# Kernel optimization log

Measured on AMD Instinct MI355X. Metric: run time of the kernel, lower is better.

## Reference

```python
import jax, jax.numpy as jnp
import numpy as np

B, CIN, COUT, S1, S2, M1, M2 = 16, 64, 64, 128, 128, 16, 16


def _cas(L, dtype):
    # Hartley 'cas' matrix: cos(2*pi*k*k'/L) + sin(2*pi*k*k'/L), symmetric LxL
    k = jnp.arange(L, dtype=dtype)
    ang = (2.0 * jnp.pi / L) * (k[:, None] * k[None, :])
    return jnp.cos(ang) + jnp.sin(ang)


def dht2(x):
    # x: [B, C, M, N] -> dense 2D discrete Hartley transform via matmuls
    M, N = x.shape[-2], x.shape[-1]
    cas_row = _cas(M, x.dtype)
    cas_col = _cas(N, x.dtype)
    # torch: matmul(x, cas_col.T) then matmul(cas_row.T, .)
    y = jnp.einsum('bimn,gn->bimg', x, cas_col)
    return jnp.einsum('mf,bimn->bifn', cas_row, y)


def idht2(x):
    return dht2(x) / (x.shape[-2] * x.shape[-1])


def _neg_freq(a):
    # roll(flip(a, [-1,-2]), (1,1), [-1,-2])
    return jnp.roll(jnp.flip(a, axis=(-2, -1)), shift=(1, 1), axis=(-2, -1))


def compl_mul2d(x1, x2):
    x1n = _neg_freq(x1)
    x2n = _neg_freq(x2)
    e = lambda a, b: jnp.einsum('bixy,ioxy->boxy', a, b)
    return 0.5 * (e(x1, x2) - e(x1n, x2n) + e(x1, x2n) + e(x1n, x2))


def setup_inputs() -> dict:
    key = jax.random.key(0)
    k1, k2, k3 = jax.random.split(key, 3)
    scale = 1.0 / (CIN * COUT)
    x = jax.random.normal(k1, (B, CIN, S1, S2), dtype=jnp.float32)
    weights1 = scale * jax.random.uniform(k2, (CIN, COUT, M1, M2), dtype=jnp.float32)
    weights2 = scale * jax.random.uniform(k3, (CIN, COUT, M1, M2), dtype=jnp.float32)
    return {'x': x, 'weights1': weights1, 'weights2': weights2}


def reference(x, weights1, weights2):
    m1, m2 = weights1.shape[2], weights1.shape[3]
    b, cout = x.shape[0], weights1.shape[1]
    s1, s2 = x.shape[-2], x.shape[-1]

    cos_part = dht2(x)
    sin_part = dht2(jnp.flip(x, axis=(-2, -1)))
    # torch.angle(complex(cos, sin)) == atan2(sin, cos)
    phase = jnp.arctan2(sin_part, cos_part)

    out_dht = jnp.zeros((b, cout, s1, s2), dtype=x.dtype)
    out_dht = out_dht.at[:, :, :m1, :m2].set(
        compl_mul2d(cos_part[:, :, :m1, :m2], weights1))
    out_dht = out_dht.at[:, :, -m1:, :m2].set(
        compl_mul2d(cos_part[:, :, -m1:, :m2], weights2))

    y = idht2(out_dht)
    return y * jnp.cos(phase)
```

## Files before the change

kernel.cpp:

```cpp
#include <hip/hip_runtime.h>

typedef _Float16 f16;
typedef f16 f16x4 __attribute__((ext_vector_type(4)));
typedef f16 f16x8 __attribute__((ext_vector_type(8)));
typedef float f32x4 __attribute__((ext_vector_type(4)));

#define LSCALE 2048.0f
#define LINV   4.8828125e-4f
#define XSX 136
#define XSW 140

#define MFMA(A,B,C) __builtin_amdgcn_mfma_f32_16x16x32_f16(A, B, C, 0, 0, 0)

__device__ __forceinline__ int frag_slot(int row, int k) {
    return ((((row >> 4) * 4 + (k >> 5)) * 64) + ((k >> 3) & 3) * 16 + (row & 15)) * 8 + (k & 7);
}

__global__ void k_cas(float* __restrict__ casf,
                      f16* __restrict__ FAh, f16* __restrict__ FAl,
                      f16* __restrict__ FVh, f16* __restrict__ FVl) {
    int f = blockIdx.x, m = threadIdx.x;
    const float SC = (float)(6.283185307179586 / 128.0);
    float ang = SC * (float)(f * m);
    double a = (double)ang;
    float v = (float)cos(a) + (float)sin(a);
    casf[f * 128 + m] = v;
    f16 h = (f16)v;
    f16 lo = (f16)((v - (float)h) * LSCALE);
    int sA = frag_slot(f, m);
    FAh[sA] = h;
    FAl[sA] = lo;
    int sV = frag_slot(f, 127 - m);
    FVh[sV] = h;
    FVl[sV] = lo;
}

__global__ __launch_bounds__(512, 2) void k_dht(
    const float* __restrict__ xg,
    const f16* __restrict__ FAh, const f16* __restrict__ FAl,
    const f16* __restrict__ FVh, const f16* __restrict__ FVl,
    float* __restrict__ outbuf,
    float* __restrict__ cp1, float* __restrict__ cp2)
{
    __shared__ __align__(16) char smem[71680];
    f16* Xh  = (f16*)smem;
    f16* Xl  = (f16*)(smem + 34816);
    f16* W1h = (f16*)smem;
    f16* W1l = (f16*)(smem + 17920);
    f16* W2h = (f16*)(smem + 35840);
    f16* W2l = (f16*)(smem + 53760);

    const int img = blockIdx.x;
    const int gh  = blockIdx.y;
    const float* X = xg + (size_t)img * 16384;
    const int t = threadIdx.x;
    const int lane = t & 63;
    const int wv = t >> 6;
    const int l15 = lane & 15;
    const int a4 = lane >> 4;

    #pragma unroll
    for (int it = 0; it < 8; ++it) {
        int i = it * 512 + t;
        int r = i >> 5, c0 = (i & 31) * 4;
        float4 xv = *(const float4*)&X[r * 128 + c0];
        const float* xp = (const float*)&xv;
        f16x4 hv, lv;
        #pragma unroll
        for (int j = 0; j < 4; ++j) {
            f16 h = (f16)xp[j];
            hv[j] = h;
            lv[j] = (f16)((xp[j] - (float)h) * LSCALE);
        }
        *(f16x4*)&Xh[r * XSX + c0] = hv;
        *(f16x4*)&Xl[r * XSX + c0] = lv;
    }
    __syncthreads();

    const int gq = wv >> 2, mq = wv & 3;
    const int Gq = 2 * gh + gq;
    f32x4 w1hi[2][2], w1lo[2][2], w2hi[2][2], w2lo[2][2];
    #pragma unroll
    for (int i = 0; i < 2; ++i)
        #pragma unroll
        for (int j = 0; j < 2; ++j) {
            w1hi[i][j] = (f32x4){0.f,0.f,0.f,0.f}; w1lo[i][j] = (f32x4){0.f,0.f,0.f,0.f};
            w2hi[i][j] = (f32x4){0.f,0.f,0.f,0.f}; w2lo[i][j] = (f32x4){0.f,0.f,0.f,0.f};
        }
    {
        #pragma unroll 1
        for (int ks = 0; ks < 4; ++ks) {
            f16x8 tah[2], tal[2], tvh[2], tvl[2];
            #pragma unroll
            for (int gt = 0; gt < 2; ++gt) {
                const int toff = (((2 * Gq + gt) * 4 + ks) * 64 + lane) * 8;
                tah[gt] = *(const f16x8*)&FAh[toff];
                tal[gt] = *(const f16x8*)&FAl[toff];
                tvh[gt] = *(const f16x8*)&FVh[toff];
                tvl[gt] = *(const f16x8*)&FVl[toff];
            }
            #pragma unroll
            for (int mt = 0; mt < 2; ++mt) {
                const int base = (32 * mq + 16 * mt + l15) * XSX + ks * 32 + 8 * a4;
                f16x8 xh = *(const f16x8*)&Xh[base];
                f16x8 xl = *(const f16x8*)&Xl[base];
                #pragma unroll
                for (int gt = 0; gt < 2; ++gt) {
                    w1hi[gt][mt] = MFMA(tah[gt], xh, w1hi[gt][mt]);
                    w1lo[gt][mt] = MFMA(tal[gt], xh, w1lo[gt][mt]);
                    w1lo[gt][mt] = MFMA(tah[gt], xl, w1lo[gt][mt]);
                    w2hi[gt][mt] = MFMA(tvh[gt], xh, w2hi[gt][mt]);
                    w2lo[gt][mt] = MFMA(tvl[gt], xh, w2lo[gt][mt]);
                    w2lo[gt][mt] = MFMA(tvh[gt], xl, w2lo[gt][mt]);
                }
            }
        }
    }
    __syncthreads();

    {
        #pragma unroll
        for (int gt = 0; gt < 2; ++gt)
            #pragma unroll
            for (int mt = 0; mt < 2; ++mt) {
                const int m = 32 * mq + 16 * mt + l15;
                #pragma unroll
                for (int r = 0; r < 4; ++r) {
                    const int g = 32 * gq + 16 * gt + 4 * a4 + r;
                    float v1 = w1hi[gt][mt][r] + LINV * w1lo[gt][mt][r];
                    f16 h1 = (f16)v1;
                    float v2 = w2hi[gt][mt][r] + LINV * w2lo[gt][mt][r];
                    f16 h2 = (f16)v2;
                    W2h[g * XSW + m] = h2;
                    W2l[g * XSW + m] = (f16)((v2 - (float)h2) * LSCALE);
                    W1h[g * XSW + m] = h1;
                    W1l[g * XSW + m] = (f16)((v1 - (float)h1) * LSCALE);
                }
            }
    }
    __syncthreads();

    const int fq = wv >> 1, gq2 = wv & 1;
    f32x4 chi[2][2], clo[2][2], shi[2][2], slo[2][2];
    #pragma unroll
    for (int i = 0; i < 2; ++i)
        #pragma unroll
        for (int j = 0; j < 2; ++j) {
            chi[i][j] = (f32x4){0.f,0.f,0.f,0.f}; clo[i][j] = (f32x4){0.f,0.f,0.f,0.f};
            shi[i][j] = (f32x4){0.f,0.f,0.f,0.f}; slo[i][j] = (f32x4){0.f,0.f,0.f,0.f};
        }
    {
        #pragma unroll 1
        for (int ks = 0; ks < 4; ++ks) {
            f16x8 tah[2], tal[2], tvh[2], tvl[2];
            #pragma unroll
            for (int ft = 0; ft < 2; ++ft) {
                const int toff = (((2 * fq + ft) * 4 + ks) * 64 + lane) * 8;
                tah[ft] = *(const f16x8*)&FAh[toff];
                tal[ft] = *(const f16x8*)&FAl[toff];
                tvh[ft] = *(const f16x8*)&FVh[toff];
                tvl[ft] = *(const f16x8*)&FVl[toff];
            }
            #pragma unroll
            for (int gt = 0; gt < 2; ++gt) {
                const int wb = (32 * gq2 + 16 * gt + l15) * XSW + ks * 32 + 8 * a4;
                f16x4 a0 = *(const f16x4*)&W1h[wb];
                f16x4 a1 = *(const f16x4*)&W1h[wb + 4];
                f16x4 b0 = *(const f16x4*)&W1l[wb];
                f16x4 b1 = *(const f16x4*)&W1l[wb + 4];
                f16x4 c0 = *(const f16x4*)&W2h[wb];
                f16x4 c1 = *(const f16x4*)&W2h[wb + 4];
                f16x4 d0 = *(const f16x4*)&W2l[wb];
                f16x4 d1 = *(const f16x4*)&W2l[wb + 4];
                f16x8 u1h = __builtin_shufflevector(a0, a1, 0,1,2,3,4,5,6,7);
                f16x8 u1l = __builtin_shufflevector(b0, b1, 0,1,2,3,4,5,6,7);
                f16x8 u2h = __builtin_shufflevector(c0, c1, 0,1,2,3,4,5,6,7);
                f16x8 u2l = __builtin_shufflevector(d0, d1, 0,1,2,3,4,5,6,7);
                #pragma unroll
                for (int ft = 0; ft < 2; ++ft) {
                    chi[ft][gt] = MFMA(tah[ft], u1h, chi[ft][gt]);
                    clo[ft][gt] = MFMA(tal[ft], u1h, clo[ft][gt]);
                    clo[ft][gt] = MFMA(tah[ft], u1l, clo[ft][gt]);
                    shi[ft][gt] = MFMA(tvh[ft], u2h, shi[ft][gt]);
                    slo[ft][gt] = MFMA(tvl[ft], u2h, slo[ft][gt]);
                    slo[ft][gt] = MFMA(tvh[ft], u2l, slo[ft][gt]);
                }
            }
        }
    }

    f16* cph = (f16*)(outbuf + (size_t)img * 16384);
    #pragma unroll
    for (int ft = 0; ft < 2; ++ft)
        #pragma unroll
        for (int gt = 0; gt < 2; ++gt) {
            const int g = 64 * gh + 32 * gq2 + 16 * gt + l15;
            #pragma unroll
            for (int r = 0; r < 4; ++r) {
                const int f = 32 * fq + 16 * ft + 4 * a4 + r;
                float Cv = chi[ft][gt][r] + LINV * clo[ft][gt][r];
                float Sv = shi[ft][gt][r] + LINV * slo[ft][gt][r];
                float d = Cv * Cv + Sv * Sv;
                float cp = (d > 0.f) ? Cv * rsqrtf(d) : 1.0f;
                cph[f * 128 + g] = (f16)cp;
                if (gh == 0 && gq2 == 0 && gt == 0) {
                    if (fq == 0 && ft == 0)
                        cp1[img * 256 + f * 16 + l15] = Cv;
                    else if (fq == 3 && ft == 1)
                        cp2[img * 256 + (f - 112) * 16 + l15] = Cv;
                }
            }
        }
}

__global__ __launch_bounds__(256) void k_inv(
    const float* __restrict__ cp1, const float* __restrict__ cp2,
    const float* __restrict__ w1,  const float* __restrict__ w2,
    const float* __restrict__ cas,
    float* __restrict__ out)
{
    __shared__ float odS[32 * 16];
    __shared__ float casF[128 * 33];
    __shared__ float Rs[128 * 17];
    __shared__ float casG[16 * 128];

    const int img = blockIdx.x;
    const int b = img >> 6, o = img & 63;
    const int t = threadIdx.x;
    const int grp = t >> 5, lane = t & 31;
    const int s2 = lane * 4;

    const f16* phg = (const f16*)(out + (size_t)img * 16384);
    f16x4 phv[16];
    #pragma unroll
    for (int r = 0; r < 16; ++r)
        phv[r] = *(const f16x4*)&phg[(grp * 16 + r) * 128 + s2];

    {
        const int xx = t >> 4, yy = t & 15;
        const int nx = (16 - xx) & 15, ny = (16 - yy) & 15;
        const int pf = xx * 16 + yy, pn = nx * 16 + ny;
        float a1p = 0.f, a1m = 0.f, a2p = 0.f, a2m = 0.f;
        #pragma unroll 4
        for (int i = 0; i < 64; ++i) {
            const int cb = (b * 64 + i) * 256;
            const int wb = (i * 64 + o) * 256;
            float A1  = cp1[cb + pf];
            float A1n = cp1[cb + pn];
            float W1v = w1[wb + pf];
            float W1n = w1[wb + pn];
            a1p = fmaf(A1,  W1v + W1n, a1p);
            a1m = fmaf(A1n, W1v - W1n, a1m);
            float A2  = cp2[cb + pf];
            float A2n = cp2[cb + pn];
            float W2v = w2[wb + pf];
            float W2n = w2[wb + pn];
            a2p = fmaf(A2,  W2v + W2n, a2p);
            a2m = fmaf(A2n, W2v - W2n, a2m);
        }
        odS[pf]       = 0.5f * (a1p + a1m);
        odS[256 + pf] = 0.5f * (a2p + a2m);
    }

    #pragma unroll
    for (int k = 0; k < 16; ++k) {
        int idx = t + k * 256;
        int s = idx >> 5, j = idx & 31;
        int f = (j < 16) ? j : (96 + j);
        casF[s * 33 + j] = cas[s * 128 + f];
    }
    #pragma unroll
    for (int k = 0; k < 8; ++k) {
        int idx = t + k * 256;
        casG[idx] = cas[idx];
    }
    __syncthreads();

    {
        const int s1 = t >> 1, gb = (t & 1) * 8;
        float acc[8];
        #pragma unroll
        for (int l = 0; l < 8; ++l) acc[l] = 0.f;
        #pragma unroll 4
        for (int j = 0; j < 32; ++j) {
            float cf = casF[s1 * 33 + j];
            #pragma unroll
            for (int l = 0; l < 8; ++l)
                acc[l] = fmaf(cf, odS[j * 16 + gb + l], acc[l]);
        }
        #pragma unroll
        for (int l = 0; l < 8; ++l) Rs[s1 * 17 + gb + l] = acc[l];
    }
    __syncthreads();

    const float inv = 1.0f / 16384.0f;
    #pragma unroll
    for (int r = 0; r < 16; ++r) {
        const int s1 = grp * 16 + r;
        float4 acc = {0.f, 0.f, 0.f, 0.f};
        #pragma unroll
        for (int g = 0; g < 16; ++g) {
            float rv = Rs[s1 * 17 + g];
            float4 c4 = *(const float4*)&casG[g * 128 + s2];
            acc.x = fmaf(rv, c4.x, acc.x);
            acc.y = fmaf(rv, c4.y, acc.y);
            acc.z = fmaf(rv, c4.z, acc.z);
            acc.w = fmaf(rv, c4.w, acc.w);
        }
        size_t idx = (size_t)img * 16384 + (size_t)s1 * 128 + s2;
        float4 res;
        res.x = acc.x * inv * (float)phv[r][0];
        res.y = acc.y * inv * (float)phv[r][1];
        res.z = acc.z * inv * (float)phv[r][2];
        res.w = acc.w * inv * (float)phv[r][3];
        *(float4*)&out[idx] = res;
    }
}

extern "C" void kernel_launch(void* const* d_in, const int* in_sizes, int n_in,
                              void* d_out, int out_size, void* d_ws, size_t ws_size,
                              hipStream_t stream) {
    (void)in_sizes; (void)n_in; (void)out_size; (void)ws_size;
    const float* x  = (const float*)d_in[0];
    const float* w1 = (const float*)d_in[1];
    const float* w2 = (const float*)d_in[2];
    float* out = (float*)d_out;
    float* ws  = (float*)d_ws;

    float* casf = ws;
    f16* FAh = (f16*)(ws + 16384);
    f16* FAl = FAh + 16384;
    f16* FVh = FAl + 16384;
    f16* FVl = FVh + 16384;
    float* cp1 = (float*)(FVl + 16384);
    float* cp2 = cp1 + 262144;

    k_cas<<<dim3(128), dim3(128), 0, stream>>>(casf, FAh, FAl, FVh, FVl);
    k_dht<<<dim3(1024, 2), dim3(512), 0, stream>>>(x, FAh, FAl, FVh, FVl, out, cp1, cp2);
    k_inv<<<dim3(1024), dim3(256), 0, stream>>>(cp1, cp2, w1, w2, casf, out);
}
```

Before: 150.5 us.

## Store pre-negated frequency copies and vectorise spectral mixing with warp specialisation

Result: slower. 164.1 us (+9.0%).

```diff
diff --git a/kernel.cpp b/kernel.cpp
--- a/kernel.cpp
+++ b/kernel.cpp
@@ -40,7 +40,8 @@
     const f16* __restrict__ FAh, const f16* __restrict__ FAl,
     const f16* __restrict__ FVh, const f16* __restrict__ FVl,
     float* __restrict__ outbuf,
-    float* __restrict__ cp1, float* __restrict__ cp2)
+    float* __restrict__ cp1, float* __restrict__ cp2,
+    float* __restrict__ cp1n, float* __restrict__ cp2n)
 {
     __shared__ __align__(16) char smem[71680];
     f16* Xh  = (f16*)smem;
@@ -204,10 +205,15 @@
                 float cp = (d > 0.f) ? Cv * rsqrtf(d) : 1.0f;
                 cph[f * 128 + g] = (f16)cp;
                 if (gh == 0 && gq2 == 0 && gt == 0) {
-                    if (fq == 0 && ft == 0)
+                    const int gn = (16 - l15) & 15;
+                    if (fq == 0 && ft == 0) {
                         cp1[img * 256 + f * 16 + l15] = Cv;
-                    else if (fq == 3 && ft == 1)
-                        cp2[img * 256 + (f - 112) * 16 + l15] = Cv;
+                        cp1n[img * 256 + ((16 - f) & 15) * 16 + gn] = Cv;
+                    } else if (fq == 3 && ft == 1) {
+                        const int fl = f - 112;
+                        cp2[img * 256 + fl * 16 + l15] = Cv;
+                        cp2n[img * 256 + ((16 - fl) & 15) * 16 + gn] = Cv;
+                    }
                 }
             }
         }
@@ -215,6 +221,7 @@
 
 __global__ __launch_bounds__(256) void k_inv(
     const float* __restrict__ cp1, const float* __restrict__ cp2,
+    const float* __restrict__ cp1n, const float* __restrict__ cp2n,
     const float* __restrict__ w1,  const float* __restrict__ w2,
     const float* __restrict__ cas,
     float* __restrict__ out)
@@ -236,43 +243,58 @@
     for (int r = 0; r < 16; ++r)
         phv[r] = *(const f16x4*)&phg[(grp * 16 + r) * 128 + s2];
 
-    {
-        const int xx = t >> 4, yy = t & 15;
-        const int nx = (16 - xx) & 15, ny = (16 - yy) & 15;
-        const int pf = xx * 16 + yy, pn = nx * 16 + ny;
-        float a1p = 0.f, a1m = 0.f, a2p = 0.f, a2m = 0.f;
+    if (t < 128) {
+        const int c  = t >> 6;
+        const int s  = t & 63;
+        const int xx = s >> 2;
+        const int yb = (s & 3) * 4;
+        const int pix = xx * 16 + yb;
+        const int nx = (16 - xx) & 15;
+        const int nlo = nx * 16 + (12 - yb);
+        const int nup = nx * 16 + ((16 - yb) & 15);
+        const float* cp  = c ? cp2  : cp1;
+        const float* cpn = c ? cp2n : cp1n;
+        const float* w   = c ? w2   : w1;
+        float4 accp = {0.f,0.f,0.f,0.f}, accm = {0.f,0.f,0.f,0.f};
         #pragma unroll 4
         for (int i = 0; i < 64; ++i) {
             const int cb = (b * 64 + i) * 256;
             const int wb = (i * 64 + o) * 256;
-            float A1  = cp1[cb + pf];
-            float A1n = cp1[cb + pn];
-            float W1v = w1[wb + pf];
-            float W1n = w1[wb + pn];
-            a1p = fmaf(A1,  W1v + W1n, a1p);
-            a1m = fmaf(A1n, W1v - W1n, a1m);
-            float A2  = cp2[cb + pf];
-            float A2n = cp2[cb + pn];
-            float W2v = w2[wb + pf];
-            float W2n = w2[wb + pn];
-            a2p = fmaf(A2,  W2v + W2n, a2p);
-            a2m = fmaf(A2n, W2v - W2n, a2m);
-        }
-        odS[pf]       = 0.5f * (a1p + a1m);
-        odS[256 + pf] = 0.5f * (a2p + a2m);
-    }
-
-    #pragma unroll
-    for (int k = 0; k < 16; ++k) {
-        int idx = t + k * 256;
-        int s = idx >> 5, j = idx & 31;
-        int f = (j < 16) ? j : (96 + j);
-        casF[s * 33 + j] = cas[s * 128 + f];
-    }
-    #pragma unroll
-    for (int k = 0; k < 8; ++k) {
-        int idx = t + k * 256;
-        casG[idx] = cas[idx];
+            float4 A4  = *(const float4*)&cp[cb + pix];
+            float4 An4 = *(const float4*)&cpn[cb + pix];
+            float4 W4  = *(const float4*)&w[wb + pix];
+            float4 lo  = *(const float4*)&w[wb + nlo];
+            float4 up  = *(const float4*)&w[wb + nup];
+            float4 Wn4 = { up.x, lo.w, lo.z, lo.y };
+            accp.x = fmaf(A4.x,  W4.x + Wn4.x, accp.x);
+            accm.x = fmaf(An4.x, W4.x - Wn4.x, accm.x);
+            accp.y = fmaf(A4.y,  W4.y + Wn4.y, accp.y);
+            accm.y = fmaf(An4.y, W4.y - Wn4.y, accm.y);
+            accp.z = fmaf(A4.z,  W4.z + Wn4.z, accp.z);
+            accm.z = fmaf(An4.z, W4.z - Wn4.z, accm.z);
+            accp.w = fmaf(A4.w,  W4.w + Wn4.w, accp.w);
+            accm.w = fmaf(An4.w, W4.w - Wn4.w, accm.w);
+        }
+        float4 od;
+        od.x = 0.5f * (accp.x + accm.x);
+        od.y = 0.5f * (accp.y + accm.y);
+        od.z = 0.5f * (accp.z + accm.z);
+        od.w = 0.5f * (accp.w + accm.w);
+        *(float4*)&odS[c * 256 + pix] = od;
+    } else {
+        const int tt = t - 128;
+        #pragma unroll
+        for (int k = 0; k < 32; ++k) {
+            int idx = tt + k * 128;
+            int s = idx >> 5, j = idx & 31;
+            int f = (j < 16) ? j : (96 + j);
+            casF[s * 33 + j] = cas[s * 128 + f];
+        }
+        #pragma unroll
+        for (int k = 0; k < 16; ++k) {
+            int idx = tt + k * 128;
+            casG[idx] = cas[idx];
+        }
     }
     __syncthreads();
 
@@ -332,10 +354,13 @@
     f16* FAl = FAh + 16384;
     f16* FVh = FAl + 16384;
     f16* FVl = FVh + 16384;
-    float* cp1 = (float*)(FVl + 16384);
-    float* cp2 = cp1 + 262144;
+    float* cp1  = (float*)(FVl + 16384);
+    float* cp2  = cp1 + 262144;
+    float* cp1n = cp2 + 262144;
+    float* cp2n = cp1n + 262144;
 
     k_cas<<<dim3(128), dim3(128), 0, stream>>>(casf, FAh, FAl, FVh, FVl);
-    k_dht<<<dim3(1024, 2), dim3(512), 0, stream>>>(x, FAh, FAl, FVh, FVl, out, cp1, cp2);
-    k_inv<<<dim3(1024), dim3(256), 0, stream>>>(cp1, cp2, w1, w2, casf, out);
-}
+    k_dht<<<dim3(1024, 2), dim3(512), 0, stream>>>(x, FAh, FAl, FVh, FVl, out,
+                                                   cp1, cp2, cp1n, cp2n);
+    k_inv<<<dim3(1024), dim3(256), 0, stream>>>(cp1, cp2, cp1n, cp2n, w1, w2, casf, out);
+}
```
